# Kernel tuning notes

Hardware: AMD Instinct MI355X
Metric: run time of the kernel (lower is better)

## Reference

```python
import jax, jax.numpy as jnp
import numpy as np

B, N, D, H, NW = 16, 400, 256, 8, 4
DH = D // H
EPS_LN = 1e-5

def _layer_norm(x, g, b):
    m = jnp.mean(x, axis=-1, keepdims=True)
    v = jnp.mean((x - m) ** 2, axis=-1, keepdims=True)
    return (x - m) / jnp.sqrt(v + EPS_LN) * g + b

def setup_inputs() -> dict:
    key = jax.random.key(0)
    ks = jax.random.split(key, 10)
    p = lambda k, shape: (jax.random.normal(k, shape, jnp.float32) * 0.02)
    return {
        'x': jax.random.normal(ks[0], (B, N, D), jnp.float32),
        'attention_weights': jax.random.normal(ks[1], (B, NW, N, N), jnp.float32),
        'Wq': p(ks[2], (D, D)), 'bq': jnp.zeros((D,), jnp.float32),
        'Wk': p(ks[3], (D, D)), 'bk': jnp.zeros((D,), jnp.float32),
        'Wv': p(ks[4], (D, D)), 'bv': jnp.zeros((D,), jnp.float32),
        'Wo': p(ks[5], (D, D)), 'bo': jnp.zeros((D,), jnp.float32),
        'g1': jnp.ones((D,), jnp.float32), 'beta1': jnp.zeros((D,), jnp.float32),
        'W1': p(ks[6], (4 * D, D)), 'b1': jnp.zeros((4 * D,), jnp.float32),
        'W2': p(ks[7], (D, 4 * D)), 'b2': jnp.zeros((D,), jnp.float32),
        'g2': jnp.ones((D,), jnp.float32), 'beta2': jnp.zeros((D,), jnp.float32),
    }

def reference(x, attention_weights, Wq, bq, Wk, bk, Wv, bv, Wo, bo,
              g1, beta1, W1, b1, W2, b2, g2, beta2):
    b, n, d = x.shape
    # QKV projections, split heads: [B, H, N, DH]
    q = (x @ Wq.T + bq).reshape(b, n, H, DH).transpose(0, 2, 1, 3)
    k = (x @ Wk.T + bk).reshape(b, n, H, DH).transpose(0, 2, 1, 3)
    v = (x @ Wv.T + bv).reshape(b, n, H, DH).transpose(0, 2, 1, 3)
    qk = jnp.einsum('bhnd,bhmd->bhnm', q, k) / np.sqrt(DH)  # [B,H,N,N]
    # signed attention averaged over the NW per-sample weight matrices
    nw = attention_weights.shape[1]
    scores = jnp.zeros_like(qk)
    for i in range(nw):  # small fixed count, not a data dim
        w = attention_weights[:, i][:, None, :, :]  # [B,1,N,N]
        s = qk * w
        e = jnp.exp(jnp.abs(s))
        scores = scores + jnp.sign(s) * e / (jnp.sum(e, axis=-1, keepdims=True) + 1e-10)
    scores = scores / nw
    attn_out = jnp.einsum('bhnm,bhmd->bhnd', scores, v)
    attn_out = attn_out.transpose(0, 2, 1, 3).reshape(b, n, d)
    attn_out = attn_out @ Wo.T + bo
    h = _layer_norm(x + attn_out, g1, beta1)
    ffn = jax.nn.relu(h @ W1.T + b1) @ W2.T + b2
    y = _layer_norm(h + ffn, g2, beta2)
    return (y, scores)
```

## Files before the change

kernel.cpp:

```cpp
#include <hip/hip_runtime.h>
#include <hip/hip_fp16.h>

typedef unsigned int uint32;

#define B_ 16
#define N_ 400
#define D_ 256
#define H_ 8
#define DH_ 32
#define NW_ 4

#if __has_builtin(__builtin_amdgcn_exp2f)
#define EXP2(x) __builtin_amdgcn_exp2f(x)
#else
#define EXP2(x) exp2f(x)
#endif

#define QK_SCL 0.2550348f

using bf16x8 = __attribute__((ext_vector_type(8))) short;
using f16x8  = __attribute__((ext_vector_type(8))) _Float16;
using f16x4  = __attribute__((ext_vector_type(4))) _Float16;
using f32x4  = __attribute__((ext_vector_type(4))) float;

__device__ __forceinline__ ushort f2b(float f) {
  uint32 u = __float_as_uint(f);
  uint32 r = (u + 0x7fffu + ((u >> 16) & 1u)) >> 16;
  return (ushort)r;
}

__global__ __launch_bounds__(256) void convert_kernel(
    const float* __restrict__ x,  const float* __restrict__ wq,
    const float* __restrict__ wk, const float* __restrict__ wv,
    const float* __restrict__ wo, const float* __restrict__ w1,
    const float* __restrict__ w2,
    ushort* __restrict__ xb,  ushort* __restrict__ wqb,
    ushort* __restrict__ wkb, ushort* __restrict__ wvb,
    ushort* __restrict__ wob, ushort* __restrict__ w1b,
    ushort* __restrict__ w2b) {
  int gid = blockIdx.x * 256 + threadIdx.x;
  const float* src; ushort* dst;
  if      (gid < 409600) { src = x;  dst = xb;  }
  else if ((gid -= 409600) < 16384) { src = wq; dst = wqb; }
  else if ((gid -= 16384) < 16384)  { src = wk; dst = wkb; }
  else if ((gid -= 16384) < 16384)  { src = wv; dst = wvb; }
  else if ((gid -= 16384) < 16384)  { src = wo; dst = wob; }
  else if ((gid -= 16384) < 65536)  { src = w1; dst = w1b; }
  else { gid -= 65536; src = w2; dst = w2b; }
  float4 f = ((const float4*)src)[gid];
  ushort4 u;
  u.x = f2b(f.x); u.y = f2b(f.y); u.z = f2b(f.z); u.w = f2b(f.w);
  *(ushort4*)&dst[(size_t)gid * 4] = u;
}

template <int RELU, int RESID, int OUT_F32, int OUT_BF16>
__global__ __launch_bounds__(256) void gemm_bt(
    const ushort* __restrict__ A, const ushort* __restrict__ W,
    const float* __restrict__ bias, const float* __restrict__ resid,
    float* __restrict__ outf, ushort* __restrict__ outb,
    int M, int N, int K) {
  __shared__ __align__(16) ushort As[2][64 * 40];
  __shared__ __align__(16) ushort Ws[2][64 * 40];
  int t = threadIdx.x;
  int l = t & 63, w = t >> 6;
  int n0 = blockIdx.x * 64, m0 = blockIdx.y * 64;
  int srow = t >> 2, sc = (t & 3) * 8;
  int lrow = l & 15, lk = (l >> 4) * 8;

  const uint4* ag = (const uint4*)&A[(size_t)(m0 + srow) * K + sc];
  const uint4* wg = (const uint4*)&W[(size_t)(n0 + srow) * K + sc];
  uint4 ar = ag[0], wr = wg[0];
  int nk = K >> 5;

  f32x4 acc[4];
#pragma unroll
  for (int nt = 0; nt < 4; nt++) acc[nt] = {0.f, 0.f, 0.f, 0.f};

  for (int kk = 0; kk < nk; kk++) {
    int cur = kk & 1;
    *(uint4*)&As[cur][srow * 40 + sc] = ar;
    *(uint4*)&Ws[cur][srow * 40 + sc] = wr;
    if (kk + 1 < nk) { ar = ag[(size_t)(kk + 1) * 4]; wr = wg[(size_t)(kk + 1) * 4]; }
    __syncthreads();
    bf16x8 af = *(const bf16x8*)&As[cur][(16 * w + lrow) * 40 + lk];
#pragma unroll
    for (int nt = 0; nt < 4; nt++) {
      bf16x8 bf = *(const bf16x8*)&Ws[cur][(nt * 16 + lrow) * 40 + lk];
      acc[nt] = __builtin_amdgcn_mfma_f32_16x16x32_bf16(af, bf, acc[nt], 0, 0, 0);
    }
  }

#pragma unroll
  for (int nt = 0; nt < 4; nt++) {
    int n = n0 + nt * 16 + lrow;
    float bv = bias[n];
#pragma unroll
    for (int r = 0; r < 4; r++) {
      int m = m0 + 16 * w + (l >> 4) * 4 + r;
      float v = acc[nt][r] + bv;
      if (RELU)  v = fmaxf(v, 0.f);
      if (RESID) v += resid[(size_t)m * N + n];
      if (OUT_F32)  outf[(size_t)m * N + n] = v;
      if (OUT_BF16) outb[(size_t)m * N + n] = f2b(v);
    }
  }
}

template <int OUT_BF16>
__global__ __launch_bounds__(512) void gemm_ln16(
    const ushort* __restrict__ A, const ushort* __restrict__ W,
    const float* __restrict__ bias, const float* __restrict__ resid,
    const float* __restrict__ g, const float* __restrict__ be,
    float* __restrict__ outf, ushort* __restrict__ outb, int K) {
  __shared__ __align__(16) ushort As[2][16 * 40];
  __shared__ __align__(16) ushort Ws[2][256 * 40];
  __shared__ float2 red[8][16];
  int t = threadIdx.x;
  int l = t & 63, w = t >> 6;
  int m0 = blockIdx.x * 16;
  int lrow = l & 15, lk = (l >> 4) * 8, lq = l >> 4;
  int srow = t >> 2, sc = (t & 3) * 8;
  int nk = K >> 5;

  const uint4* ag  = (const uint4*)&A[(size_t)(m0 + srow) * K + sc];
  const uint4* wg0 = (const uint4*)&W[(size_t)srow * K + sc];
  const uint4* wg1 = (const uint4*)&W[(size_t)(128 + srow) * K + sc];

  uint4 ar = {0, 0, 0, 0};
  if (t < 64) ar = ag[0];
  uint4 w0 = wg0[0], w1 = wg1[0];

  f32x4 acc[2];
  acc[0] = {0.f, 0.f, 0.f, 0.f};
  acc[1] = {0.f, 0.f, 0.f, 0.f};

  for (int kk = 0; kk < nk; kk++) {
    int cur = kk & 1;
    if (t < 64) *(uint4*)&As[cur][srow * 40 + sc] = ar;
    *(uint4*)&Ws[cur][srow * 40 + sc]         = w0;
    *(uint4*)&Ws[cur][(128 + srow) * 40 + sc] = w1;
    if (kk + 1 < nk) {
      size_t off = (size_t)(kk + 1) * 4;
      if (t < 64) ar = ag[off];
      w0 = wg0[off]; w1 = wg1[off];
    }
    __syncthreads();
    bf16x8 af = *(const bf16x8*)&As[cur][lrow * 40 + lk];
#pragma unroll
    for (int fc = 0; fc < 2; fc++) {
      bf16x8 bf = *(const bf16x8*)&Ws[cur][(w * 32 + fc * 16 + lrow) * 40 + lk];
      acc[fc] = __builtin_amdgcn_mfma_f32_16x16x32_bf16(af, bf, acc[fc], 0, 0, 0);
    }
    __syncthreads();
  }

  float s[4], ss[4];
#pragma unroll
  for (int r = 0; r < 4; r++) { s[r] = 0.f; ss[r] = 0.f; }
#pragma unroll
  for (int fc = 0; fc < 2; fc++) {
    int n = w * 32 + fc * 16 + lrow;
    float bv = bias[n];
#pragma unroll
    for (int r = 0; r < 4; r++) {
      int m = m0 + lq * 4 + r;
      float v = acc[fc][r] + bv + resid[(size_t)m * 256 + n];
      acc[fc][r] = v;
      s[r] += v;
      ss[r] += v * v;
    }
  }
#pragma unroll
  for (int o = 1; o <= 8; o <<= 1) {
#pragma unroll
    for (int r = 0; r < 4; r++) {
      s[r] += __shfl_xor(s[r], o);
      ss[r] += __shfl_xor(ss[r], o);
    }
  }
  if (lrow == 0) {
#pragma unroll
    for (int r = 0; r < 4; r++) red[w][lq * 4 + r] = {s[r], ss[r]};
  }
  __syncthreads();

#pragma unroll
  for (int r = 0; r < 4; r++) {
    int row = lq * 4 + r;
    float sum = 0.f, sq = 0.f;
#pragma unroll
    for (int ww = 0; ww < 8; ww++) {
      float2 p = red[ww][row];
      sum += p.x; sq += p.y;
    }
    float mean = sum * (1.f / 256.f);
    float var = sq * (1.f / 256.f) - mean * mean;
    float rinv = rsqrtf(var + 1e-5f);
    int m = m0 + row;
#pragma unroll
    for (int fc = 0; fc < 2; fc++) {
      int n = w * 32 + fc * 16 + lrow;
      float y = (acc[fc][r] - mean) * rinv * g[n] + be[n];
      outf[(size_t)m * 256 + n] = y;
      if (OUT_BF16) outb[(size_t)m * 256 + n] = f2b(y);
    }
  }
}

__global__ __launch_bounds__(256) void qkv_gemm(
    const ushort* __restrict__ xb, const ushort* __restrict__ wq,
    const ushort* __restrict__ wk, const ushort* __restrict__ wv,
    const float* __restrict__ bq, const float* __restrict__ bk,
    const float* __restrict__ bv,
    _Float16* __restrict__ qh, _Float16* __restrict__ kh,
    _Float16* __restrict__ vt) {
  __shared__ __align__(16) ushort As[2][64 * 40];
  __shared__ __align__(16) ushort Ws[2][64 * 40];
  int z = blockIdx.z;
  const ushort* W = (z == 0) ? wq : (z == 1) ? wk : wv;
  const float* bias = (z == 0) ? bq : (z == 1) ? bk : bv;

  int t = threadIdx.x;
  int l = t & 63, w = t >> 6;
  int n0 = blockIdx.x * 64, m0 = blockIdx.y * 64;
  int srow = t >> 2, sc = (t & 3) * 8;
  int lrow = l & 15, lk = (l >> 4) * 8;

  const uint4* ag = (const uint4*)&xb[(size_t)(m0 + srow) * 256 + sc];
  const uint4* wg = (const uint4*)&W[(size_t)(n0 + srow) * 256 + sc];
  uint4 ar = ag[0], wr = wg[0];

  f32x4 acc[4];
#pragma unroll
  for (int nt = 0; nt < 4; nt++) acc[nt] = {0.f, 0.f, 0.f, 0.f};

  for (int kk = 0; kk < 8; kk++) {
    int cur = kk & 1;
    *(uint4*)&As[cur][srow * 40 + sc] = ar;
    *(uint4*)&Ws[cur][srow * 40 + sc] = wr;
    if (kk + 1 < 8) { ar = ag[(kk + 1) * 4]; wr = wg[(kk + 1) * 4]; }
    __syncthreads();
    bf16x8 af = *(const bf16x8*)&As[cur][(16 * w + lrow) * 40 + lk];
#pragma unroll
    for (int nt = 0; nt < 4; nt++) {
      bf16x8 bf = *(const bf16x8*)&Ws[cur][(nt * 16 + lrow) * 40 + lk];
      acc[nt] = __builtin_amdgcn_mfma_f32_16x16x32_bf16(af, bf, acc[nt], 0, 0, 0);
    }
  }

  int mb = m0 + 16 * w + (l >> 4) * 4;
  int bb = mb / 400;
  int mi = mb - bb * 400;
#pragma unroll
  for (int nt = 0; nt < 4; nt++) {
    int n = n0 + nt * 16 + lrow;
    float bvv = bias[n];
    if (z < 2) {
      _Float16* out = z ? kh : qh;
      float scl = z ? 1.f : QK_SCL;
      int hh = n >> 5, dd = n & 31;
      _Float16* dst = out + (((size_t)(bb * 8 + hh)) * 400 + mi) * 32 + dd;
#pragma unroll
      for (int r = 0; r < 4; r++)
        dst[(size_t)r * 32] = (_Float16)((acc[nt][r] + bvv) * scl);
    } else {
      _Float16 h4[4];
#pragma unroll
      for (int r = 0; r < 4; r++) h4[r] = (_Float16)(acc[nt][r] + bvv);
      *(uint2*)&vt[((size_t)bb * 256 + n) * 400 + mi] = *(uint2*)h4;
    }
  }
}

#define SP 416

__global__ __launch_bounds__(256, 4) void attn_kernel(
    const _Float16* __restrict__ qh, const _Float16* __restrict__ kh,
    const _Float16* __restrict__ vt, const float* __restrict__ aw,
    float* __restrict__ scores, ushort* __restrict__ attnb) {
  __shared__ __align__(16) char smem[16 * SP * 2];
  __half* S = (__half*)smem;

  int id = blockIdx.x;
  int c = ((id >> 6) << 3) | (id & 7);
  int hh = (id >> 3) & 7;
  int b = c / 25;
  int n0 = (c - b * 25) * 16;

  int t = threadIdx.x;
  int w = t >> 6, l = t & 63;
  int lq = l >> 4, lr = l & 15;

  {
    const _Float16* qbase = qh + (((size_t)(b * 8 + hh)) * 400 + n0) * 32;
    const _Float16* kbase = kh + ((size_t)(b * 8 + hh)) * 400 * 32;
    f16x8 af = *(const f16x8*)(qbase + lr * 32 + lq * 8);
    for (int mt = w; mt < 25; mt += 4) {
      f16x8 bf = *(const f16x8*)(kbase + (size_t)(mt * 16 + lr) * 32 + lq * 8);
      f32x4 cc = {0.f, 0.f, 0.f, 0.f};
      cc = __builtin_amdgcn_mfma_f32_16x16x32_f16(af, bf, cc, 0, 0, 0);
#pragma unroll
      for (int r = 0; r < 4; r++)
        S[(lq * 4 + r) * SP + mt * 16 + lr] = __float2half(cc[r]);
    }
  }
  __syncthreads();

  {
    int m0 = l * 4, m1 = 256 + l * 4;
    bool act = (l < 36);
    int m1c = act ? m1 : m0;
    const float* awb = aw + (((size_t)(b * 4)) * 400 + n0) * 400;
    float* scb = scores + (((size_t)(b * 8 + hh)) * 400 + n0) * 400;

    float4 A0[4], A1[4], B0[4], B1[4];
    {
      const float* awn = awb + (size_t)w * 400;
#pragma unroll
      for (int i = 0; i < 4; i++) {
        A0[i] = *(const float4*)(awn + (size_t)i * 160000 + m0);
        A1[i] = *(const float4*)(awn + (size_t)i * 160000 + m1c);
      }
    }

    auto grp = [&](int n, float4 (&c0)[4], float4 (&c1)[4],
                   float4 (&p0)[4], float4 (&p1)[4], bool pf) {
      if (pf) {
        const float* awn = awb + (size_t)(n + 4) * 400;
#pragma unroll
        for (int i = 0; i < 4; i++) {
          p0[i] = *(const float4*)(awn + (size_t)i * 160000 + m0);
          p1[i] = *(const float4*)(awn + (size_t)i * 160000 + m1c);
        }
      }
      _Float16* srow = (_Float16*)S + (size_t)n * SP;
      float* scout = scb + (size_t)n * 400;

      f16x4 s0 = *(const f16x4*)(srow + m0);
      float q0[4], q1[4];
#pragma unroll
      for (int j = 0; j < 4; j++) q0[j] = (float)s0[j];
      if (act) {
        f16x4 s1 = *(const f16x4*)(srow + m1);
#pragma unroll
        for (int j = 0; j < 4; j++) q1[j] = (float)s1[j];
      } else {
#pragma unroll
        for (int j = 0; j < 4; j++) q1[j] = 0.f;
      }

      f16x4 e0[4], e1[4];
      float z[4];
#pragma unroll
      for (int i = 0; i < 4; i++) {
        float zz0 = 0.f, zz1 = 0.f;
#pragma unroll
        for (int j = 0; j < 4; j++) {
          float tt = q0[j] * ((const float*)&c0[i])[j];
          float ef = EXP2(fabsf(tt));
          zz0 += ef;
          e0[i][j] = (_Float16)copysignf(ef, tt);
        }
#pragma unroll
        for (int j = 0; j < 4; j++) {
          float tt = q1[j] * ((const float*)&c1[i])[j];
          float ef = EXP2(fabsf(tt));
          zz1 += ef;
          e1[i][j] = (_Float16)copysignf(ef, tt);
        }
        z[i] = zz0 + (act ? zz1 : 0.f);
      }

#pragma unroll
      for (int o = 1; o <= 32; o <<= 1) {
#pragma unroll
        for (int i = 0; i < 4; i++) z[i] += __shfl_xor(z[i], o);
      }

      f16x4 o0, o1;
#pragma unroll
      for (int j = 0; j < 4; j++) { o0[j] = (_Float16)0.f; o1[j] = (_Float16)0.f; }
#pragma unroll
      for (int i = 0; i < 4; i++) {
        _Float16 zh = (_Float16)(0.25f / (z[i] + 1e-10f));
        f16x4 zv = {zh, zh, zh, zh};
        o0 += e0[i] * zv;
        o1 += e1[i] * zv;
      }

      float4 so;
#pragma unroll
      for (int j = 0; j < 4; j++) ((float*)&so)[j] = (float)o0[j];
      *(float4*)(scout + m0) = so;
      *(f16x4*)(srow + m0) = o0;
      if (act) {
        float4 s1o;
#pragma unroll
        for (int j = 0; j < 4; j++) ((float*)&s1o)[j] = (float)o1[j];
        *(float4*)(scout + m1) = s1o;
        *(f16x4*)(srow + m1) = o1;
      } else if (l < 40) {
        f16x4 hz;
#pragma unroll
        for (int j = 0; j < 4; j++) hz[j] = (_Float16)0.f;
        *(f16x4*)(srow + m1) = hz;
      }
    };

    grp(w,      A0, A1, B0, B1, true);
    grp(4 + w,  B0, B1, A0, A1, true);
    grp(8 + w,  A0, A1, B0, B1, true);
    grp(12 + w, B0, B1, A0, A1, false);
  }
  __syncthreads();

  const _Float16* vbase = vt + (((size_t)b) * 256 + hh * 32) * 400;
  f32x4 a0 = {0.f, 0.f, 0.f, 0.f}, a1 = {0.f, 0.f, 0.f, 0.f};
  const _Float16* Sh = (const _Float16*)S;
  for (int c2 = w; c2 < 13; c2 += 4) {
    f16x8 sf = *(const f16x8*)(Sh + lr * SP + c2 * 32 + lq * 8);
    f16x8 v0 = *(const f16x8*)(vbase + (size_t)lr * 400 + c2 * 32 + lq * 8);
    f16x8 v1 = *(const f16x8*)(vbase + (size_t)(16 + lr) * 400 + c2 * 32 + lq * 8);
    a0 = __builtin_amdgcn_mfma_f32_16x16x32_f16(sf, v0, a0, 0, 0, 0);
    a1 = __builtin_amdgcn_mfma_f32_16x16x32_f16(sf, v1, a1, 0, 0, 0);
  }
  __syncthreads();
  float* Of = (float*)smem;
#pragma unroll
  for (int r = 0; r < 4; r++) {
    Of[(w * 16 + lq * 4 + r) * 32 + lr] = a0[r];
    Of[(w * 16 + lq * 4 + r) * 32 + 16 + lr] = a1[r];
  }
  __syncthreads();
  for (int o = t; o < 512; o += 256) {
    int n = o >> 5, d = o & 31;
    float s = Of[n * 32 + d] + Of[512 + n * 32 + d] +
              Of[1024 + n * 32 + d] + Of[1536 + n * 32 + d];
    attnb[((size_t)(b * 400 + n0 + n)) * 256 + hh * 32 + d] = f2b(s);
  }
}

extern "C" void kernel_launch(void* const* d_in, const int* in_sizes, int n_in,
                              void* d_out, int out_size, void* d_ws,
                              size_t ws_size, hipStream_t stream) {
  const float* x   = (const float*)d_in[0];
  const float* aw  = (const float*)d_in[1];
  const float* Wq  = (const float*)d_in[2];
  const float* bq  = (const float*)d_in[3];
  const float* Wk  = (const float*)d_in[4];
  const float* bk  = (const float*)d_in[5];
  const float* Wv  = (const float*)d_in[6];
  const float* bv  = (const float*)d_in[7];
  const float* Wo  = (const float*)d_in[8];
  const float* bo  = (const float*)d_in[9];
  const float* g1  = (const float*)d_in[10];
  const float* be1 = (const float*)d_in[11];
  const float* W1  = (const float*)d_in[12];
  const float* b1  = (const float*)d_in[13];
  const float* W2  = (const float*)d_in[14];
  const float* b2  = (const float*)d_in[15];
  const float* g2  = (const float*)d_in[16];
  const float* be2 = (const float*)d_in[17];

  if (ws_size < 34340864) return;

  char* ws = (char*)d_ws;
  ushort*   xb    = (ushort*)(ws + 0);
  ushort*   wqb   = (ushort*)(ws + 3276800);
  ushort*   wkb   = (ushort*)(ws + 3407872);
  ushort*   wvb   = (ushort*)(ws + 3538944);
  ushort*   wob   = (ushort*)(ws + 3670016);
  ushort*   w1b   = (ushort*)(ws + 3801088);
  ushort*   w2b   = (ushort*)(ws + 4325376);
  _Float16* qhb   = (_Float16*)(ws + 4849664);
  _Float16* khb   = (_Float16*)(ws + 8126464);
  _Float16* vtb   = (_Float16*)(ws + 11403264);
  ushort*   attnb = (ushort*)(ws + 14680064);
  float*    ao    = (float*)(ws + 17956864);
  float*    hbuf  = (float*)(ws + 24510464);
  ushort*   hb    = (ushort*)(ws + 31064064);
  ushort*   ffn1b = (ushort*)qhb;
  (void)ao;

  float* yout   = (float*)d_out;
  float* scores = yout + 1638400;

  convert_kernel<<<2368, 256, 0, stream>>>(x, Wq, Wk, Wv, Wo, W1, W2,
                                           xb, wqb, wkb, wvb, wob, w1b, w2b);
  qkv_gemm<<<dim3(4, 100, 3), 256, 0, stream>>>(
      xb, wqb, wkb, wvb, bq, bk, bv, qhb, khb, vtb);
  attn_kernel<<<3200, 256, 0, stream>>>(qhb, khb, vtb, aw, scores, attnb);
  gemm_ln16<1><<<400, 512, 0, stream>>>(attnb, wob, bo, x, g1, be1,
                                        hbuf, hb, 256);
  gemm_bt<1, 0, 0, 1><<<dim3(16, 100), 256, 0, stream>>>(
      hb, w1b, b1, nullptr, nullptr, ffn1b, 6400, 1024, 256);
  gemm_ln16<0><<<400, 512, 0, stream>>>(ffn1b, w2b, b2, hbuf, g2, be2,
                                        yout, nullptr, 1024);
}
```

Baseline: 243.6 us.

## Fuse output projection, LN1, FFN and LN2 into one per-row-tile tail kernel

Replaces the three tail launches (Wo GEMM+LN1, FFN1 GEMM with ReLU, FFN2 GEMM+LN2) with one kernel in which each 512-thread block owns 16 rows. The block keeps h (fp32 and bf16) and the 16x1024 FFN hidden activations in LDS instead of writing them to global memory and reading them back. This removes the global round-trips and two launches, but each block now streams all of Wo, W1 and W2 itself, and the larger LDS footprint (about 100KB) lowers occupancy. The grid is only 400 blocks.

```diff
diff --git a/kernel.cpp b/kernel.cpp
--- a/kernel.cpp
+++ b/kernel.cpp
@@ -53,160 +53,6 @@
   *(ushort4*)&dst[(size_t)gid * 4] = u;
 }
 
-template <int RELU, int RESID, int OUT_F32, int OUT_BF16>
-__global__ __launch_bounds__(256) void gemm_bt(
-    const ushort* __restrict__ A, const ushort* __restrict__ W,
-    const float* __restrict__ bias, const float* __restrict__ resid,
-    float* __restrict__ outf, ushort* __restrict__ outb,
-    int M, int N, int K) {
-  __shared__ __align__(16) ushort As[2][64 * 40];
-  __shared__ __align__(16) ushort Ws[2][64 * 40];
-  int t = threadIdx.x;
-  int l = t & 63, w = t >> 6;
-  int n0 = blockIdx.x * 64, m0 = blockIdx.y * 64;
-  int srow = t >> 2, sc = (t & 3) * 8;
-  int lrow = l & 15, lk = (l >> 4) * 8;
-
-  const uint4* ag = (const uint4*)&A[(size_t)(m0 + srow) * K + sc];
-  const uint4* wg = (const uint4*)&W[(size_t)(n0 + srow) * K + sc];
-  uint4 ar = ag[0], wr = wg[0];
-  int nk = K >> 5;
-
-  f32x4 acc[4];
-#pragma unroll
-  for (int nt = 0; nt < 4; nt++) acc[nt] = {0.f, 0.f, 0.f, 0.f};
-
-  for (int kk = 0; kk < nk; kk++) {
-    int cur = kk & 1;
-    *(uint4*)&As[cur][srow * 40 + sc] = ar;
-    *(uint4*)&Ws[cur][srow * 40 + sc] = wr;
-    if (kk + 1 < nk) { ar = ag[(size_t)(kk + 1) * 4]; wr = wg[(size_t)(kk + 1) * 4]; }
-    __syncthreads();
-    bf16x8 af = *(const bf16x8*)&As[cur][(16 * w + lrow) * 40 + lk];
-#pragma unroll
-    for (int nt = 0; nt < 4; nt++) {
-      bf16x8 bf = *(const bf16x8*)&Ws[cur][(nt * 16 + lrow) * 40 + lk];
-      acc[nt] = __builtin_amdgcn_mfma_f32_16x16x32_bf16(af, bf, acc[nt], 0, 0, 0);
-    }
-  }
-
-#pragma unroll
-  for (int nt = 0; nt < 4; nt++) {
-    int n = n0 + nt * 16 + lrow;
-    float bv = bias[n];
-#pragma unroll
-    for (int r = 0; r < 4; r++) {
-      int m = m0 + 16 * w + (l >> 4) * 4 + r;
-      float v = acc[nt][r] + bv;
-      if (RELU)  v = fmaxf(v, 0.f);
-      if (RESID) v += resid[(size_t)m * N + n];
-      if (OUT_F32)  outf[(size_t)m * N + n] = v;
-      if (OUT_BF16) outb[(size_t)m * N + n] = f2b(v);
-    }
-  }
-}
-
-template <int OUT_BF16>
-__global__ __launch_bounds__(512) void gemm_ln16(
-    const ushort* __restrict__ A, const ushort* __restrict__ W,
-    const float* __restrict__ bias, const float* __restrict__ resid,
-    const float* __restrict__ g, const float* __restrict__ be,
-    float* __restrict__ outf, ushort* __restrict__ outb, int K) {
-  __shared__ __align__(16) ushort As[2][16 * 40];
-  __shared__ __align__(16) ushort Ws[2][256 * 40];
-  __shared__ float2 red[8][16];
-  int t = threadIdx.x;
-  int l = t & 63, w = t >> 6;
-  int m0 = blockIdx.x * 16;
-  int lrow = l & 15, lk = (l >> 4) * 8, lq = l >> 4;
-  int srow = t >> 2, sc = (t & 3) * 8;
-  int nk = K >> 5;
-
-  const uint4* ag  = (const uint4*)&A[(size_t)(m0 + srow) * K + sc];
-  const uint4* wg0 = (const uint4*)&W[(size_t)srow * K + sc];
-  const uint4* wg1 = (const uint4*)&W[(size_t)(128 + srow) * K + sc];
-
-  uint4 ar = {0, 0, 0, 0};
-  if (t < 64) ar = ag[0];
-  uint4 w0 = wg0[0], w1 = wg1[0];
-
-  f32x4 acc[2];
-  acc[0] = {0.f, 0.f, 0.f, 0.f};
-  acc[1] = {0.f, 0.f, 0.f, 0.f};
-
-  for (int kk = 0; kk < nk; kk++) {
-    int cur = kk & 1;
-    if (t < 64) *(uint4*)&As[cur][srow * 40 + sc] = ar;
-    *(uint4*)&Ws[cur][srow * 40 + sc]         = w0;
-    *(uint4*)&Ws[cur][(128 + srow) * 40 + sc] = w1;
-    if (kk + 1 < nk) {
-      size_t off = (size_t)(kk + 1) * 4;
-      if (t < 64) ar = ag[off];
-      w0 = wg0[off]; w1 = wg1[off];
-    }
-    __syncthreads();
-    bf16x8 af = *(const bf16x8*)&As[cur][lrow * 40 + lk];
-#pragma unroll
-    for (int fc = 0; fc < 2; fc++) {
-      bf16x8 bf = *(const bf16x8*)&Ws[cur][(w * 32 + fc * 16 + lrow) * 40 + lk];
-      acc[fc] = __builtin_amdgcn_mfma_f32_16x16x32_bf16(af, bf, acc[fc], 0, 0, 0);
-    }
-    __syncthreads();
-  }
-
-  float s[4], ss[4];
-#pragma unroll
-  for (int r = 0; r < 4; r++) { s[r] = 0.f; ss[r] = 0.f; }
-#pragma unroll
-  for (int fc = 0; fc < 2; fc++) {
-    int n = w * 32 + fc * 16 + lrow;
-    float bv = bias[n];
-#pragma unroll
-    for (int r = 0; r < 4; r++) {
-      int m = m0 + lq * 4 + r;
-      float v = acc[fc][r] + bv + resid[(size_t)m * 256 + n];
-      acc[fc][r] = v;
-      s[r] += v;
-      ss[r] += v * v;
-    }
-  }
-#pragma unroll
-  for (int o = 1; o <= 8; o <<= 1) {
-#pragma unroll
-    for (int r = 0; r < 4; r++) {
-      s[r] += __shfl_xor(s[r], o);
-      ss[r] += __shfl_xor(ss[r], o);
-    }
-  }
-  if (lrow == 0) {
-#pragma unroll
-    for (int r = 0; r < 4; r++) red[w][lq * 4 + r] = {s[r], ss[r]};
-  }
-  __syncthreads();
-
-#pragma unroll
-  for (int r = 0; r < 4; r++) {
-    int row = lq * 4 + r;
-    float sum = 0.f, sq = 0.f;
-#pragma unroll
-    for (int ww = 0; ww < 8; ww++) {
-      float2 p = red[ww][row];
-      sum += p.x; sq += p.y;
-    }
-    float mean = sum * (1.f / 256.f);
-    float var = sq * (1.f / 256.f) - mean * mean;
-    float rinv = rsqrtf(var + 1e-5f);
-    int m = m0 + row;
-#pragma unroll
-    for (int fc = 0; fc < 2; fc++) {
-      int n = w * 32 + fc * 16 + lrow;
-      float y = (acc[fc][r] - mean) * rinv * g[n] + be[n];
-      outf[(size_t)m * 256 + n] = y;
-      if (OUT_BF16) outb[(size_t)m * 256 + n] = f2b(y);
-    }
-  }
-}
-
 __global__ __launch_bounds__(256) void qkv_gemm(
     const ushort* __restrict__ xb, const ushort* __restrict__ wq,
     const ushort* __restrict__ wk, const ushort* __restrict__ wv,
@@ -437,6 +283,193 @@
     float s = Of[n * 32 + d] + Of[512 + n * 32 + d] +
               Of[1024 + n * 32 + d] + Of[1536 + n * 32 + d];
     attnb[((size_t)(b * 400 + n0 + n)) * 256 + hh * 32 + d] = f2b(s);
+  }
+}
+
+__global__ __launch_bounds__(512) void tail_kernel(
+    const ushort* __restrict__ attnb, const float* __restrict__ x,
+    const ushort* __restrict__ wo, const float* __restrict__ bo,
+    const float* __restrict__ g1, const float* __restrict__ be1,
+    const ushort* __restrict__ w1, const float* __restrict__ b1,
+    const ushort* __restrict__ w2, const float* __restrict__ b2,
+    const float* __restrict__ g2, const float* __restrict__ be2,
+    float* __restrict__ yout) {
+  __shared__ __align__(16) ushort Ws[2][256 * 40];
+  __shared__ __align__(16) ushort ha[16 * 264];
+  __shared__ __align__(16) ushort hbl[16 * 264];
+  __shared__ __align__(16) float  hf[16 * 256];
+  __shared__ __align__(16) ushort f1l[16 * 1032];
+  __shared__ float2 red[8][16];
+
+  int t = threadIdx.x;
+  int l = t & 63, w = t >> 6;
+  int lrow = l & 15, lq = l >> 4;
+  int m0 = blockIdx.x * 16;
+  int srow = t >> 1, sc = (t & 1) * 16;
+  int nc0 = w * 32 + lrow, nc1 = nc0 + 16;
+
+  {
+    int arow = t >> 5, ac = (t & 31) * 8;
+    *(uint4*)&ha[arow * 264 + ac] =
+        *(const uint4*)&attnb[(size_t)(m0 + arow) * 256 + ac];
+  }
+
+  f32x4 acc0 = {0.f, 0.f, 0.f, 0.f}, acc1 = {0.f, 0.f, 0.f, 0.f};
+  {
+    uint4 r0 = *(const uint4*)&wo[(size_t)srow * 256 + sc];
+    uint4 r1 = *(const uint4*)&wo[(size_t)srow * 256 + sc + 8];
+    __syncthreads();
+    for (int kk = 0; kk < 8; kk++) {
+      int cur = kk & 1;
+      *(uint4*)&Ws[cur][srow * 40 + sc] = r0;
+      *(uint4*)&Ws[cur][srow * 40 + sc + 8] = r1;
+      if (kk + 1 < 8) {
+        r0 = *(const uint4*)&wo[(size_t)srow * 256 + (kk + 1) * 32 + sc];
+        r1 = *(const uint4*)&wo[(size_t)srow * 256 + (kk + 1) * 32 + sc + 8];
+      }
+      __syncthreads();
+      bf16x8 af = *(const bf16x8*)&ha[lrow * 264 + kk * 32 + lq * 8];
+      bf16x8 b0 = *(const bf16x8*)&Ws[cur][nc0 * 40 + lq * 8];
+      bf16x8 b1f = *(const bf16x8*)&Ws[cur][nc1 * 40 + lq * 8];
+      acc0 = __builtin_amdgcn_mfma_f32_16x16x32_bf16(af, b0, acc0, 0, 0, 0);
+      acc1 = __builtin_amdgcn_mfma_f32_16x16x32_bf16(af, b1f, acc1, 0, 0, 0);
+      __syncthreads();
+    }
+  }
+  {
+    float bv0 = bo[nc0], bv1 = bo[nc1];
+    float v0[4], v1[4], s[4], ss[4];
+#pragma unroll
+    for (int r = 0; r < 4; r++) {
+      int m = m0 + lq * 4 + r;
+      v0[r] = acc0[r] + bv0 + x[(size_t)m * 256 + nc0];
+      v1[r] = acc1[r] + bv1 + x[(size_t)m * 256 + nc1];
+      s[r] = v0[r] + v1[r];
+      ss[r] = v0[r] * v0[r] + v1[r] * v1[r];
+    }
+#pragma unroll
+    for (int o = 1; o <= 8; o <<= 1)
+#pragma unroll
+      for (int r = 0; r < 4; r++) {
+        s[r] += __shfl_xor(s[r], o);
+        ss[r] += __shfl_xor(ss[r], o);
+      }
+    if (lrow == 0)
+#pragma unroll
+      for (int r = 0; r < 4; r++) red[w][lq * 4 + r] = {s[r], ss[r]};
+    __syncthreads();
+#pragma unroll
+    for (int r = 0; r < 4; r++) {
+      int row = lq * 4 + r;
+      float sum = 0.f, sq = 0.f;
+#pragma unroll
+      for (int ww = 0; ww < 8; ww++) {
+        float2 p = red[ww][row];
+        sum += p.x; sq += p.y;
+      }
+      float mean = sum * (1.f / 256.f);
+      float var = sq * (1.f / 256.f) - mean * mean;
+      float rinv = rsqrtf(var + 1e-5f);
+      float y0 = (v0[r] - mean) * rinv * g1[nc0] + be1[nc0];
+      float y1 = (v1[r] - mean) * rinv * g1[nc1] + be1[nc1];
+      hf[row * 256 + nc0] = y0;
+      hf[row * 256 + nc1] = y1;
+      hbl[row * 264 + nc0] = f2b(y0);
+      hbl[row * 264 + nc1] = f2b(y1);
+    }
+  }
+  __syncthreads();
+
+  for (int nb = 0; nb < 4; nb++) {
+    f32x4 ac0 = {0.f, 0.f, 0.f, 0.f}, ac1 = {0.f, 0.f, 0.f, 0.f};
+    const ushort* wb = w1 + (size_t)(nb * 256) * 256;
+    uint4 r0 = *(const uint4*)&wb[(size_t)srow * 256 + sc];
+    uint4 r1 = *(const uint4*)&wb[(size_t)srow * 256 + sc + 8];
+    for (int kk = 0; kk < 8; kk++) {
+      int cur = kk & 1;
+      *(uint4*)&Ws[cur][srow * 40 + sc] = r0;
+      *(uint4*)&Ws[cur][srow * 40 + sc + 8] = r1;
+      if (kk + 1 < 8) {
+        r0 = *(const uint4*)&wb[(size_t)srow * 256 + (kk + 1) * 32 + sc];
+        r1 = *(const uint4*)&wb[(size_t)srow * 256 + (kk + 1) * 32 + sc + 8];
+      }
+      __syncthreads();
+      bf16x8 af = *(const bf16x8*)&hbl[lrow * 264 + kk * 32 + lq * 8];
+      bf16x8 b0 = *(const bf16x8*)&Ws[cur][nc0 * 40 + lq * 8];
+      bf16x8 b1f = *(const bf16x8*)&Ws[cur][nc1 * 40 + lq * 8];
+      ac0 = __builtin_amdgcn_mfma_f32_16x16x32_bf16(af, b0, ac0, 0, 0, 0);
+      ac1 = __builtin_amdgcn_mfma_f32_16x16x32_bf16(af, b1f, ac1, 0, 0, 0);
+      __syncthreads();
+    }
+    float bv0 = b1[nb * 256 + nc0], bv1 = b1[nb * 256 + nc1];
+#pragma unroll
+    for (int r = 0; r < 4; r++) {
+      int row = lq * 4 + r;
+      f1l[row * 1032 + nb * 256 + nc0] = f2b(fmaxf(ac0[r] + bv0, 0.f));
+      f1l[row * 1032 + nb * 256 + nc1] = f2b(fmaxf(ac1[r] + bv1, 0.f));
+    }
+  }
+  __syncthreads();
+
+  f32x4 cc0 = {0.f, 0.f, 0.f, 0.f}, cc1 = {0.f, 0.f, 0.f, 0.f};
+  {
+    uint4 r0 = *(const uint4*)&w2[(size_t)srow * 1024 + sc];
+    uint4 r1 = *(const uint4*)&w2[(size_t)srow * 1024 + sc + 8];
+    for (int kk = 0; kk < 32; kk++) {
+      int cur = kk & 1;
+      *(uint4*)&Ws[cur][srow * 40 + sc] = r0;
+      *(uint4*)&Ws[cur][srow * 40 + sc + 8] = r1;
+      if (kk + 1 < 32) {
+        r0 = *(const uint4*)&w2[(size_t)srow * 1024 + (kk + 1) * 32 + sc];
+        r1 = *(const uint4*)&w2[(size_t)srow * 1024 + (kk + 1) * 32 + sc + 8];
+      }
+      __syncthreads();
+      bf16x8 af = *(const bf16x8*)&f1l[lrow * 1032 + kk * 32 + lq * 8];
+      bf16x8 b0 = *(const bf16x8*)&Ws[cur][nc0 * 40 + lq * 8];
+      bf16x8 b1f = *(const bf16x8*)&Ws[cur][nc1 * 40 + lq * 8];
+      cc0 = __builtin_amdgcn_mfma_f32_16x16x32_bf16(af, b0, cc0, 0, 0, 0);
+      cc1 = __builtin_amdgcn_mfma_f32_16x16x32_bf16(af, b1f, cc1, 0, 0, 0);
+      __syncthreads();
+    }
+  }
+  {
+    float bv0 = b2[nc0], bv1 = b2[nc1];
+    float v0[4], v1[4], s[4], ss[4];
+#pragma unroll
+    for (int r = 0; r < 4; r++) {
+      int row = lq * 4 + r;
+      v0[r] = cc0[r] + bv0 + hf[row * 256 + nc0];
+      v1[r] = cc1[r] + bv1 + hf[row * 256 + nc1];
+      s[r] = v0[r] + v1[r];
+      ss[r] = v0[r] * v0[r] + v1[r] * v1[r];
+    }
+#pragma unroll
+    for (int o = 1; o <= 8; o <<= 1)
+#pragma unroll
+      for (int r = 0; r < 4; r++) {
+        s[r] += __shfl_xor(s[r], o);
+        ss[r] += __shfl_xor(ss[r], o);
+      }
+    if (lrow == 0)
+#pragma unroll
+      for (int r = 0; r < 4; r++) red[w][lq * 4 + r] = {s[r], ss[r]};
+    __syncthreads();
+#pragma unroll
+    for (int r = 0; r < 4; r++) {
+      int row = lq * 4 + r;
+      float sum = 0.f, sq = 0.f;
+#pragma unroll
+      for (int ww = 0; ww < 8; ww++) {
+        float2 p = red[ww][row];
+        sum += p.x; sq += p.y;
+      }
+      float mean = sum * (1.f / 256.f);
+      float var = sq * (1.f / 256.f) - mean * mean;
+      float rinv = rsqrtf(var + 1e-5f);
+      int m = m0 + row;
+      yout[(size_t)m * 256 + nc0] = (v0[r] - mean) * rinv * g2[nc0] + be2[nc0];
+      yout[(size_t)m * 256 + nc1] = (v1[r] - mean) * rinv * g2[nc1] + be2[nc1];
+    }
   }
 }
 
@@ -476,11 +509,6 @@
   _Float16* khb   = (_Float16*)(ws + 8126464);
   _Float16* vtb   = (_Float16*)(ws + 11403264);
   ushort*   attnb = (ushort*)(ws + 14680064);
-  float*    ao    = (float*)(ws + 17956864);
-  float*    hbuf  = (float*)(ws + 24510464);
-  ushort*   hb    = (ushort*)(ws + 31064064);
-  ushort*   ffn1b = (ushort*)qhb;
-  (void)ao;
 
   float* yout   = (float*)d_out;
   float* scores = yout + 1638400;
@@ -490,10 +518,6 @@
   qkv_gemm<<<dim3(4, 100, 3), 256, 0, stream>>>(
       xb, wqb, wkb, wvb, bq, bk, bv, qhb, khb, vtb);
   attn_kernel<<<3200, 256, 0, stream>>>(qhb, khb, vtb, aw, scores, attnb);
-  gemm_ln16<1><<<400, 512, 0, stream>>>(attnb, wob, bo, x, g1, be1,
-                                        hbuf, hb, 256);
-  gemm_bt<1, 0, 0, 1><<<dim3(16, 100), 256, 0, stream>>>(
-      hb, w1b, b1, nullptr, nullptr, ffn1b, 6400, 1024, 256);
-  gemm_ln16<0><<<400, 512, 0, stream>>>(ffn1b, w2b, b2, hbuf, g2, be2,
-                                        yout, nullptr, 1024);
+  tail_kernel<<<400, 512, 0, stream>>>(attnb, x, wob, bo, g1, be1,
+                                       w1b, b1, w2b, b2, g2, be2, yout);
 }
```

Result: slower. 263.2 us (+8.0%).
